# Performance work log

Hardware: AMD Instinct MI355X
Metric: run time of the kernel (lower is better)

## Reference

```python
import jax, jax.numpy as jnp
import numpy as np

B, S, D, H, A = 2, 2048, 1024, 16, 64
INIT_STD = 0.02


def setup_inputs() -> dict:
    key = jax.random.key(0)
    ks = jax.random.split(key, 5)
    return {
        "residual": jax.random.normal(ks[0], (B, S, D), dtype=jnp.float32),
        "Wq": jax.random.normal(ks[1], (H, D, A), dtype=jnp.float32) * INIT_STD,
        "Wk": jax.random.normal(ks[2], (H, D, A), dtype=jnp.float32) * INIT_STD,
        "Wv": jax.random.normal(ks[3], (H, D, A), dtype=jnp.float32) * INIT_STD,
        "Wo": jax.random.normal(ks[4], (H, A, D), dtype=jnp.float32) * INIT_STD,
        "bq": jnp.zeros((H, A), dtype=jnp.float32),
        "bk": jnp.zeros((H, A), dtype=jnp.float32),
        "bv": jnp.zeros((H, A), dtype=jnp.float32),
        "bo": jnp.zeros((D,), dtype=jnp.float32),
    }


def reference(residual, Wq, Wk, Wv, Wo, bq, bk, bv, bo):
    # residual: [B,S,D]; W{q,k,v}: [H,D,A]; Wo: [H,A,D]
    q = jnp.einsum("bsd,hda->bhsa", residual, Wq) + bq[None, :, None, :]
    k = jnp.einsum("bsd,hda->bhsa", residual, Wk) + bk[None, :, None, :]
    v = jnp.einsum("bsd,hda->bhsa", residual, Wv) + bv[None, :, None, :]
    scale = 1.0 / jnp.sqrt(jnp.float32(q.shape[-1]))
    scores = jnp.einsum("bhsa,bhta->bhst", q, k) * scale  # [B,H,S,S]
    s = scores.shape[-1]
    causal = jnp.tril(jnp.ones((s, s), dtype=bool))  # True = keep
    # original masked_fill with -100000.0 (not -inf); stay faithful
    masked = jnp.where(causal, scores, jnp.float32(-100000.0))
    pattern = jax.nn.softmax(masked, axis=-1)
    z = jnp.einsum("bhst,bhta->bshа".replace("а", "a"), pattern, v)  # [B,S,H,A]
    out = jnp.einsum("bsha,had->bsd", z, Wo) + bo
    return out
```

## Files before the change

kernel.cpp:

```cpp
#include <hip/hip_runtime.h>
#include <hip/hip_bf16.h>

#define B_ 2
#define S_ 2048
#define D_ 1024
#define H_ 16
#define A_ 64

typedef __attribute__((ext_vector_type(8))) short bf16x8;
typedef __attribute__((ext_vector_type(4))) float f32x4;
typedef __attribute__((ext_vector_type(4))) unsigned int u32x4;
typedef __attribute__((ext_vector_type(2))) unsigned int u32x2;

#define QSCALE 0.1803368801111204f

__device__ inline short f2bf(float f) {
    union { float f; unsigned u; } x; x.f = f;
    unsigned r = x.u + 0x7fff + ((x.u >> 16) & 1);
    return (short)(r >> 16);
}

__device__ __forceinline__ void gld16(const short* g, short* l) {
    __builtin_amdgcn_global_load_lds(
        (const __attribute__((address_space(1))) unsigned int*)g,
        (__attribute__((address_space(3))) unsigned int*)l, 16, 0, 0);
}

__device__ inline unsigned cvt_pk_bf16(float lo, float hi) {
    unsigned r;
    asm("v_cvt_pk_bf16_f32 %0, %1, %2" : "=v"(r) : "v"(lo), "v"(hi));
    return r;
}
__device__ inline void pl32swap(unsigned &a, unsigned &b) {
    u32x2 r = __builtin_amdgcn_permlane32_swap(a, b, false, false);
    a = r[0]; b = r[1];
}
__device__ inline void pl16swap(unsigned &a, unsigned &b) {
    u32x2 r = __builtin_amdgcn_permlane16_swap(a, b, false, false);
    a = r[0]; b = r[1];
}
__device__ inline float cross_quad_max(float x) {
    unsigned a = __builtin_bit_cast(unsigned, x), b = a;
    pl32swap(a, b);
    float y = fmaxf(__builtin_bit_cast(float, a), __builtin_bit_cast(float, b));
    unsigned c = __builtin_bit_cast(unsigned, y), d = c;
    pl16swap(c, d);
    return fmaxf(__builtin_bit_cast(float, c), __builtin_bit_cast(float, d));
}
__device__ inline float cross_quad_sum(float x) {
    unsigned a = __builtin_bit_cast(unsigned, x), b = a;
    pl32swap(a, b);
    float y = __builtin_bit_cast(float, a) + __builtin_bit_cast(float, b);
    unsigned c = __builtin_bit_cast(unsigned, y), d = c;
    pl16swap(c, d);
    return __builtin_bit_cast(float, c) + __builtin_bit_cast(float, d);
}

__global__ __launch_bounds__(256) void cast_kernel(const float* __restrict__ x,
                                                   short* __restrict__ y, int n) {
    int i = (blockIdx.x * 256 + threadIdx.x) * 8;
    if (i < n) {
        float4 a = *(const float4*)(x + i);
        float4 b = *(const float4*)(x + i + 4);
        bf16x8 o;
        o[0]=f2bf(a.x); o[1]=f2bf(a.y); o[2]=f2bf(a.z); o[3]=f2bf(a.w);
        o[4]=f2bf(b.x); o[5]=f2bf(b.y); o[6]=f2bf(b.z); o[7]=f2bf(b.w);
        *(bf16x8*)(y + i) = o;
    }
}

__global__ __launch_bounds__(256) void wtrans_kernel(
    const float* __restrict__ Wq, const float* __restrict__ Wk,
    const float* __restrict__ Wv, const float* __restrict__ Wo,
    short* __restrict__ Wt, short* __restrict__ Wot) {
    const int kt = blockIdx.x, yy = blockIdx.y, z = blockIdx.z;
    __shared__ short T[64 * 72];
    const int tid = threadIdx.x;
    const int r = tid >> 2, c0 = (tid & 3) * 16;
    const float* src;
    if (z < 3) {
        const float* W = z == 0 ? Wq : (z == 1 ? Wk : Wv);
        src = &W[yy * (D_ * A_) + (kt * 64 + r) * A_ + c0];
    } else {
        src = &Wo[(kt * 64 + r) * D_ + yy * 64 + c0];
    }
    #pragma unroll
    for (int q = 0; q < 4; q++) {
        float4 f = *(const float4*)(src + q * 4);
        T[r * 72 + c0 + q * 4 + 0] = f2bf(f.x);
        T[r * 72 + c0 + q * 4 + 1] = f2bf(f.y);
        T[r * 72 + c0 + q * 4 + 2] = f2bf(f.z);
        T[r * 72 + c0 + q * 4 + 3] = f2bf(f.w);
    }
    __syncthreads();
    const int a = tid >> 2, kc = (tid & 3) * 16;
    bf16x8 o0, o1;
    #pragma unroll
    for (int j = 0; j < 8; j++) {
        o0[j] = T[(kc + j) * 72 + a];
        o1[j] = T[(kc + 8 + j) * 72 + a];
    }
    const int n_base = (z < 3) ? z * 1024 + yy * 64 : yy * 64;
    short* dst = (z < 3) ? &Wt[(n_base + a) * D_ + kt * 64 + kc]
                         : &Wot[(n_base + a) * D_ + kt * 64 + kc];
    *(bf16x8*)dst = o0;
    *(bf16x8*)(dst + 8) = o1;
}

__global__ __launch_bounds__(256) void qkv_gemm(
    const short* __restrict__ X, const short* __restrict__ Wt,
    const float* __restrict__ bq, const float* __restrict__ bk, const float* __restrict__ bv,
    short* __restrict__ Qb, short* __restrict__ Kb, short* __restrict__ Vt) {
    const int mt = blockIdx.x, nt = blockIdx.y;
    const int m0 = mt * 128, n0 = nt * 128;
    const int sel = n0 >> 10;
    __shared__ short Xl[2][4096], Wl[2][4096];
    const int tid = threadIdx.x, wv = tid >> 6, lane = tid & 63, quad = lane >> 4, l16 = lane & 15;
    const int srow = tid >> 2, schunk = (tid & 3) * 8;
    f32x4 acc[4][4] = {};
    const short* pA0 = &X [(m0      + srow) * D_ + schunk];
    const short* pA1 = &X [(m0 + 64 + srow) * D_ + schunk];
    const short* pB0 = &Wt[(n0      + srow) * D_ + schunk];
    const short* pB1 = &Wt[(n0 + 64 + srow) * D_ + schunk];

    #define QSTAGE(bu, off) do { \
        gld16(pA0 + (off), &Xl[bu][tid * 8]); \
        gld16(pA1 + (off), &Xl[bu][2048 + tid * 8]); \
        gld16(pB0 + (off), &Wl[bu][tid * 8]); \
        gld16(pB1 + (off), &Wl[bu][2048 + tid * 8]); \
    } while (0)

    QSTAGE(0, 0);
    __syncthreads();
    const int rm = (wv & 1) * 64, cn = (wv >> 1) * 64;
    for (int i = 0; i < 32; i++) {
        const int bu = i & 1;
        if (i < 31) QSTAGE(bu ^ 1, (i + 1) * 32);
        bf16x8 af[4];
        #pragma unroll
        for (int rt = 0; rt < 4; rt++)
            af[rt] = *(bf16x8*)&Xl[bu][(rm + rt * 16 + l16) * 32 + quad * 8];
        #pragma unroll
        for (int ct = 0; ct < 4; ct++) {
            bf16x8 bf = *(bf16x8*)&Wl[bu][(cn + ct * 16 + l16) * 32 + quad * 8];
            #pragma unroll
            for (int rt = 0; rt < 4; rt++)
                acc[rt][ct] = __builtin_amdgcn_mfma_f32_16x16x32_bf16(af[rt], bf, acc[rt][ct], 0, 0, 0);
        }
        __syncthreads();
    }
    #undef QSTAGE
    const int b = m0 >> 11;
    const float* bias = sel == 0 ? bq : (sel == 1 ? bk : bv);
    if (sel < 2) {
        short* dst = sel == 0 ? Qb : Kb;
        const float scale = sel == 0 ? QSCALE : 1.0f;
        #pragma unroll
        for (int ct = 0; ct < 4; ct++) {
            const int n = n0 + cn + ct * 16 + l16;
            const int h = (n >> 6) & 15, a = n & 63;
            const float bi = bias[n & 1023];
            #pragma unroll
            for (int rt = 0; rt < 4; rt++)
                #pragma unroll
                for (int r = 0; r < 4; r++) {
                    const int row = m0 + rm + rt * 16 + quad * 4 + r;
                    const int s = row & (S_ - 1);
                    dst[(((b * H_) + h) * S_ + s) * A_ + a] = f2bf((acc[rt][ct][r] + bi) * scale);
                }
        }
    } else {
        #pragma unroll
        for (int ct = 0; ct < 4; ct++) {
            const int n = n0 + cn + ct * 16 + l16;
            const int h = (n >> 6) & 15, a = n & 63;
            const float bi = bias[n & 1023];
            #pragma unroll
            for (int rt = 0; rt < 4; rt++) {
                short4 pk;
                pk.x = f2bf(acc[rt][ct][0] + bi);
                pk.y = f2bf(acc[rt][ct][1] + bi);
                pk.z = f2bf(acc[rt][ct][2] + bi);
                pk.w = f2bf(acc[rt][ct][3] + bi);
                const int row = m0 + rm + rt * 16 + quad * 4;
                const int s = row & (S_ - 1);
                *(short4*)&Vt[(((b * H_) + h) * A_ + a) * S_ + s] = pk;
            }
        }
    }
}

__global__ __launch_bounds__(512, 4) void flash_kernel(
    const short* __restrict__ Qb, const short* __restrict__ Kb,
    const short* __restrict__ Vt, short* __restrict__ Z) {
    const int p = blockIdx.x, h = blockIdx.y, b = blockIdx.z;
    const int bh = b * H_ + h;
    const int qlo = p, qhi = 31 - p;
    __shared__ short Kl[2][4096], Vl[2][4096];
    const int tid = threadIdx.x, wv = tid >> 6, lane = tid & 63, quad = lane >> 4, l16 = lane & 15;
    const int wg = wv & 3;
    const int myqt = (wv < 4) ? qhi : qlo;
    const int qpos = wg * 16 + l16;

    const int L = tid;
    const int srow = (L >> 7) * 16 + (L & 15);
    const int scol = ((L >> 6) & 1) * 32 + ((L >> 4) & 3) * 8;

    const short* qptr = &Qb[(bh * S_ + myqt * 64 + wg * 16 + l16) * A_ + quad * 8];
    bf16x8 qf[2] = { *(const bf16x8*)qptr, *(const bf16x8*)(qptr + 32) };

    f32x4 O[4] = {};
    float m_i = -1e30f, l_i = 0.f;

    bf16x8 kreg = *(const bf16x8*)&Kb[(bh * S_ + srow) * A_ + scol];
    bf16x8 vreg = *(const bf16x8*)&Vt[(bh * A_ + srow) * S_ + scol];

    for (int kt = 0; kt <= qhi; kt++) {
        const int bu = kt & 1;
        *(bf16x8*)&Kl[bu][L * 8] = kreg;
        *(bf16x8*)&Vl[bu][L * 8] = vreg;
        __syncthreads();
        if (kt < qhi) {
            kreg = *(const bf16x8*)&Kb[(bh * S_ + (kt + 1) * 64 + srow) * A_ + scol];
            vreg = *(const bf16x8*)&Vt[(bh * A_ + srow) * S_ + (kt + 1) * 64 + scol];
        }
        if (kt <= myqt) {
            f32x4 sacc[4] = {};
            #pragma unroll
            for (int kk = 0; kk < 2; kk++)
                #pragma unroll
                for (int ct = 0; ct < 4; ct++) {
                    bf16x8 kf = *(bf16x8*)&Kl[bu][((ct * 2 + kk) * 64 + lane) * 8];
                    sacc[ct] = __builtin_amdgcn_mfma_f32_16x16x32_bf16(kf, qf[kk], sacc[ct], 0, 0, 0);
                }
            if (kt == myqt) {
                #pragma unroll
                for (int ct = 0; ct < 4; ct++)
                    #pragma unroll
                    for (int r = 0; r < 4; r++)
                        if (ct * 16 + quad * 4 + r > qpos) sacc[ct][r] = -1e30f;
            }
            f32x4 t4;
            #pragma unroll
            for (int r = 0; r < 4; r++)
                t4[r] = fmaxf(fmaxf(sacc[0][r], sacc[1][r]), fmaxf(sacc[2][r], sacc[3][r]));
            float vmax = fmaxf(fmaxf(t4[0], t4[1]), fmaxf(t4[2], t4[3]));
            vmax = cross_quad_max(vmax);
            const float mn = fmaxf(m_i, vmax);
            const float alpha = exp2f(m_i - mn);
            m_i = mn;
            #pragma unroll
            for (int ct = 0; ct < 4; ct++)
                #pragma unroll
                for (int r = 0; r < 4; r++)
                    sacc[ct][r] = exp2f(sacc[ct][r] - mn);
            f32x4 ps;
            #pragma unroll
            for (int r = 0; r < 4; r++)
                ps[r] = (sacc[0][r] + sacc[1][r]) + (sacc[2][r] + sacc[3][r]);
            float rs = (ps[0] + ps[1]) + (ps[2] + ps[3]);
            rs = cross_quad_sum(rs);
            l_i = l_i * alpha + rs;
            #pragma unroll
            for (int ct = 0; ct < 4; ct++) O[ct] *= alpha;
            #pragma unroll
            for (int kk = 0; kk < 2; kk++) {
                unsigned A0 = cvt_pk_bf16(sacc[2 * kk][0], sacc[2 * kk][1]);
                unsigned A1 = cvt_pk_bf16(sacc[2 * kk][2], sacc[2 * kk][3]);
                unsigned B0 = cvt_pk_bf16(sacc[2 * kk + 1][0], sacc[2 * kk + 1][1]);
                unsigned B1 = cvt_pk_bf16(sacc[2 * kk + 1][2], sacc[2 * kk + 1][3]);
                pl32swap(A0, B0);
                pl16swap(A0, B0);
                pl32swap(A1, B1);
                pl16swap(A1, B1);
                u32x4 wu; wu[0] = A0; wu[1] = A1; wu[2] = B0; wu[3] = B1;
                bf16x8 pb = __builtin_bit_cast(bf16x8, wu);
                #pragma unroll
                for (int ct = 0; ct < 4; ct++) {
                    bf16x8 vf = *(bf16x8*)&Vl[bu][((ct * 2 + kk) * 64 + lane) * 8];
                    O[ct] = __builtin_amdgcn_mfma_f32_16x16x32_bf16(vf, pb, O[ct], 0, 0, 0);
                }
            }
        }
    }
    const float inv = 1.0f / l_i;
    const int s = myqt * 64 + wg * 16 + l16;
    #pragma unroll
    for (int ct = 0; ct < 4; ct++) {
        short4 o4;
        o4.x = f2bf(O[ct][0] * inv);
        o4.y = f2bf(O[ct][1] * inv);
        o4.z = f2bf(O[ct][2] * inv);
        o4.w = f2bf(O[ct][3] * inv);
        *(short4*)&Z[(b * S_ + s) * (H_ * A_) + h * A_ + ct * 16 + quad * 4] = o4;
    }
}

__global__ __launch_bounds__(256) void proj_gemm(
    const short* __restrict__ Zb, const short* __restrict__ Wot,
    const float* __restrict__ bo, float* __restrict__ out) {
    const int mt = blockIdx.x, nt = blockIdx.y;
    const int m0 = mt * 128, n0 = nt * 64;
    __shared__ short Xl[2][4096], Wl[2][2048];
    const int tid = threadIdx.x, wv = tid >> 6, lane = tid & 63, quad = lane >> 4, l16 = lane & 15;
    const int srow = tid >> 2, schunk = (tid & 3) * 8;
    f32x4 acc[4][2] = {};
    const short* pA0 = &Zb [(m0      + srow) * D_ + schunk];
    const short* pA1 = &Zb [(m0 + 64 + srow) * D_ + schunk];
    const short* pB0 = &Wot[(n0      + srow) * D_ + schunk];

    #define PSTAGE(bu, off) do { \
        gld16(pA0 + (off), &Xl[bu][tid * 8]); \
        gld16(pA1 + (off), &Xl[bu][2048 + tid * 8]); \
        gld16(pB0 + (off), &Wl[bu][tid * 8]); \
    } while (0)

    PSTAGE(0, 0);
    __syncthreads();
    const int rm = (wv & 1) * 64, cn = (wv >> 1) * 32;
    for (int i = 0; i < 32; i++) {
        const int bu = i & 1;
        if (i < 31) PSTAGE(bu ^ 1, (i + 1) * 32);
        bf16x8 af[4];
        #pragma unroll
        for (int rt = 0; rt < 4; rt++)
            af[rt] = *(bf16x8*)&Xl[bu][(rm + rt * 16 + l16) * 32 + quad * 8];
        #pragma unroll
        for (int ct = 0; ct < 2; ct++) {
            bf16x8 bf = *(bf16x8*)&Wl[bu][(cn + ct * 16 + l16) * 32 + quad * 8];
            #pragma unroll
            for (int rt = 0; rt < 4; rt++)
                acc[rt][ct] = __builtin_amdgcn_mfma_f32_16x16x32_bf16(af[rt], bf, acc[rt][ct], 0, 0, 0);
        }
        __syncthreads();
    }
    #undef PSTAGE
    #pragma unroll
    for (int ct = 0; ct < 2; ct++) {
        const int n = n0 + cn + ct * 16 + l16;
        const float bi = bo[n];
        #pragma unroll
        for (int rt = 0; rt < 4; rt++)
            #pragma unroll
            for (int r = 0; r < 4; r++) {
                const int row = m0 + rm + rt * 16 + quad * 4 + r;
                out[row * D_ + n] = acc[rt][ct][r] + bi;
            }
    }
}

extern "C" void kernel_launch(void* const* d_in, const int* in_sizes, int n_in,
                              void* d_out, int out_size, void* d_ws, size_t ws_size,
                              hipStream_t stream) {
    const float* residual = (const float*)d_in[0];
    const float* Wq = (const float*)d_in[1];
    const float* Wk = (const float*)d_in[2];
    const float* Wv = (const float*)d_in[3];
    const float* Wo = (const float*)d_in[4];
    const float* bq = (const float*)d_in[5];
    const float* bk = (const float*)d_in[6];
    const float* bv = (const float*)d_in[7];
    const float* bo = (const float*)d_in[8];
    float* out = (float*)d_out;

    char* ws = (char*)d_ws;
    const size_t NE = (size_t)B_ * S_ * D_;
    short* Xbf = (short*)(ws);
    short* Wt  = (short*)(ws +  8ull * 1024 * 1024);
    short* Wot = (short*)(ws + 14ull * 1024 * 1024);
    short* Qb  = (short*)(ws + 16ull * 1024 * 1024);
    short* Kb  = (short*)(ws + 24ull * 1024 * 1024);
    short* Vt  = (short*)(ws + 32ull * 1024 * 1024);
    short* Zb  = (short*)(ws + 40ull * 1024 * 1024);

    hipLaunchKernelGGL(cast_kernel, dim3((int)(NE / (256 * 8))), dim3(256), 0, stream,
                       residual, Xbf, (int)NE);
    hipLaunchKernelGGL(wtrans_kernel, dim3(16, 16, 4), dim3(256), 0, stream,
                       Wq, Wk, Wv, Wo, Wt, Wot);
    hipLaunchKernelGGL(qkv_gemm, dim3(32, 24), dim3(256), 0, stream,
                       Xbf, Wt, bq, bk, bv, Qb, Kb, Vt);
    hipLaunchKernelGGL(flash_kernel, dim3(16, H_, B_), dim3(512), 0, stream,
                       Qb, Kb, Vt, Zb);
    hipLaunchKernelGGL(proj_gemm, dim3(32, 16), dim3(256), 0, stream,
                       Zb, Wot, bo, out);
}
```

Before: 204.1 us.

## Swizzle GEMM LDS tiles and pair adjacent query tiles in flash kernel

The QKV and output-projection GEMMs now XOR-swizzle the 16-byte chunk position within each 32-element LDS row, both when staging via global_load_lds and when reading MFMA fragments, to reduce LDS bank conflicts. The flash attention kernel now pairs adjacent query tiles (2x, 2x+1) per block instead of mirror pairs (p, 31-p). This reduces idle iterations for the lower wave group but makes per-block work uneven. Block order is reversed for half of the head/batch combinations to spread heavy blocks across the dispatch order.

```diff
diff --git a/kernel.cpp b/kernel.cpp
--- a/kernel.cpp
+++ b/kernel.cpp
@@ -116,12 +116,13 @@
     const int sel = n0 >> 10;
     __shared__ short Xl[2][4096], Wl[2][4096];
     const int tid = threadIdx.x, wv = tid >> 6, lane = tid & 63, quad = lane >> 4, l16 = lane & 15;
-    const int srow = tid >> 2, schunk = (tid & 3) * 8;
+    const int srow = tid >> 2;
+    const int csrc = (((tid & 3) ^ ((srow >> 1) & 3)) * 8);
     f32x4 acc[4][4] = {};
-    const short* pA0 = &X [(m0      + srow) * D_ + schunk];
-    const short* pA1 = &X [(m0 + 64 + srow) * D_ + schunk];
-    const short* pB0 = &Wt[(n0      + srow) * D_ + schunk];
-    const short* pB1 = &Wt[(n0 + 64 + srow) * D_ + schunk];
+    const short* pA0 = &X [(m0      + srow) * D_ + csrc];
+    const short* pA1 = &X [(m0 + 64 + srow) * D_ + csrc];
+    const short* pB0 = &Wt[(n0      + srow) * D_ + csrc];
+    const short* pB1 = &Wt[(n0 + 64 + srow) * D_ + csrc];
 
     #define QSTAGE(bu, off) do { \
         gld16(pA0 + (off), &Xl[bu][tid * 8]); \
@@ -133,16 +134,17 @@
     QSTAGE(0, 0);
     __syncthreads();
     const int rm = (wv & 1) * 64, cn = (wv >> 1) * 64;
+    const int rsw = (quad ^ ((l16 >> 1) & 3)) * 8;
     for (int i = 0; i < 32; i++) {
         const int bu = i & 1;
         if (i < 31) QSTAGE(bu ^ 1, (i + 1) * 32);
         bf16x8 af[4];
         #pragma unroll
         for (int rt = 0; rt < 4; rt++)
-            af[rt] = *(bf16x8*)&Xl[bu][(rm + rt * 16 + l16) * 32 + quad * 8];
+            af[rt] = *(bf16x8*)&Xl[bu][(rm + rt * 16 + l16) * 32 + rsw];
         #pragma unroll
         for (int ct = 0; ct < 4; ct++) {
-            bf16x8 bf = *(bf16x8*)&Wl[bu][(cn + ct * 16 + l16) * 32 + quad * 8];
+            bf16x8 bf = *(bf16x8*)&Wl[bu][(cn + ct * 16 + l16) * 32 + rsw];
             #pragma unroll
             for (int rt = 0; rt < 4; rt++)
                 acc[rt][ct] = __builtin_amdgcn_mfma_f32_16x16x32_bf16(af[rt], bf, acc[rt][ct], 0, 0, 0);
@@ -193,13 +195,14 @@
 __global__ __launch_bounds__(512, 4) void flash_kernel(
     const short* __restrict__ Qb, const short* __restrict__ Kb,
     const short* __restrict__ Vt, short* __restrict__ Z) {
-    const int p = blockIdx.x, h = blockIdx.y, b = blockIdx.z;
+    const int xx = blockIdx.x, h = blockIdx.y, b = blockIdx.z;
+    const int x = (((h >> 3) ^ b) & 1) ? (15 - xx) : xx;
     const int bh = b * H_ + h;
-    const int qlo = p, qhi = 31 - p;
+    const int qa = 2 * x, qb = 2 * x + 1;
     __shared__ short Kl[2][4096], Vl[2][4096];
     const int tid = threadIdx.x, wv = tid >> 6, lane = tid & 63, quad = lane >> 4, l16 = lane & 15;
     const int wg = wv & 3;
-    const int myqt = (wv < 4) ? qhi : qlo;
+    const int myqt = (wv < 4) ? qb : qa;
     const int qpos = wg * 16 + l16;
 
     const int L = tid;
@@ -215,12 +218,12 @@
     bf16x8 kreg = *(const bf16x8*)&Kb[(bh * S_ + srow) * A_ + scol];
     bf16x8 vreg = *(const bf16x8*)&Vt[(bh * A_ + srow) * S_ + scol];
 
-    for (int kt = 0; kt <= qhi; kt++) {
+    for (int kt = 0; kt <= qb; kt++) {
         const int bu = kt & 1;
         *(bf16x8*)&Kl[bu][L * 8] = kreg;
         *(bf16x8*)&Vl[bu][L * 8] = vreg;
         __syncthreads();
-        if (kt < qhi) {
+        if (kt < qb) {
             kreg = *(const bf16x8*)&Kb[(bh * S_ + (kt + 1) * 64 + srow) * A_ + scol];
             vreg = *(const bf16x8*)&Vt[(bh * A_ + srow) * S_ + (kt + 1) * 64 + scol];
         }
@@ -303,11 +306,12 @@
     const int m0 = mt * 128, n0 = nt * 64;
     __shared__ short Xl[2][4096], Wl[2][2048];
     const int tid = threadIdx.x, wv = tid >> 6, lane = tid & 63, quad = lane >> 4, l16 = lane & 15;
-    const int srow = tid >> 2, schunk = (tid & 3) * 8;
+    const int srow = tid >> 2;
+    const int csrc = (((tid & 3) ^ ((srow >> 1) & 3)) * 8);
     f32x4 acc[4][2] = {};
-    const short* pA0 = &Zb [(m0      + srow) * D_ + schunk];
-    const short* pA1 = &Zb [(m0 + 64 + srow) * D_ + schunk];
-    const short* pB0 = &Wot[(n0      + srow) * D_ + schunk];
+    const short* pA0 = &Zb [(m0      + srow) * D_ + csrc];
+    const short* pA1 = &Zb [(m0 + 64 + srow) * D_ + csrc];
+    const short* pB0 = &Wot[(n0      + srow) * D_ + csrc];
 
     #define PSTAGE(bu, off) do { \
         gld16(pA0 + (off), &Xl[bu][tid * 8]); \
@@ -318,16 +322,17 @@
     PSTAGE(0, 0);
     __syncthreads();
     const int rm = (wv & 1) * 64, cn = (wv >> 1) * 32;
+    const int rsw = (quad ^ ((l16 >> 1) & 3)) * 8;
     for (int i = 0; i < 32; i++) {
         const int bu = i & 1;
         if (i < 31) PSTAGE(bu ^ 1, (i + 1) * 32);
         bf16x8 af[4];
         #pragma unroll
         for (int rt = 0; rt < 4; rt++)
-            af[rt] = *(bf16x8*)&Xl[bu][(rm + rt * 16 + l16) * 32 + quad * 8];
+            af[rt] = *(bf16x8*)&Xl[bu][(rm + rt * 16 + l16) * 32 + rsw];
         #pragma unroll
         for (int ct = 0; ct < 2; ct++) {
-            bf16x8 bf = *(bf16x8*)&Wl[bu][(cn + ct * 16 + l16) * 32 + quad * 8];
+            bf16x8 bf = *(bf16x8*)&Wl[bu][(cn + ct * 16 + l16) * 32 + rsw];
             #pragma unroll
             for (int rt = 0; rt < 4; rt++)
                 acc[rt][ct] = __builtin_amdgcn_mfma_f32_16x16x32_bf16(af[rt], bf, acc[rt][ct], 0, 0, 0);
```

Result: no change. 202.8 us (-0.6%).
